# Optimization experiments

Measured on AMD Instinct MI355X. Metric: run time of the kernel, lower is better.

The kernel has to match this reference:

```python
import jax, jax.numpy as jnp
import numpy as np

B, N, DIM, H, DH = 16, 1024, 768, 12, 64
SCALE = DH ** -0.5


def setup_inputs() -> dict:
    key = jax.random.key(0)
    k1, k2, k3 = jax.random.split(key, 3)
    x = jax.random.normal(k1, (B, N, DIM), dtype=jnp.float32)
    W_qkv = jax.random.normal(k2, (DIM, 3 * H * DH), dtype=jnp.float32) * (DIM ** -0.5)
    W_out = jax.random.normal(k3, (H * DH, DIM), dtype=jnp.float32) * ((H * DH) ** -0.5)
    b_out = jnp.zeros((DIM,), dtype=jnp.float32)
    # perm = [0] + random shuffle of 1..N-1 (matches module's construction)
    rng = np.random.default_rng(0)
    perm = jnp.asarray(np.concatenate([[0], rng.permutation(np.arange(1, N))]), dtype=jnp.int32)
    return {"x": x, "W_qkv": W_qkv, "W_out": W_out, "b_out": b_out, "perm": perm}


def reference(x, W_qkv, W_out, b_out, perm):
    # QKV projection: [b, n, 3*h*d]
    qkv = jnp.einsum('bnd,de->bne', x, W_qkv)
    q, k, v = jnp.split(qkv, 3, axis=-1)
    # [b, n, h*d] -> [b, h, n, d]
    reshape = lambda t: t.reshape(B, N, H, DH).transpose(0, 2, 1, 3)
    q, k, v = reshape(q), reshape(k), reshape(v)
    # permute query rows
    q = q[:, :, perm]
    dots = jnp.einsum('bhqd,bhkd->bhqk', q, k) * SCALE
    attn = jax.nn.softmax(dots, axis=-1)
    out = jnp.einsum('bhqk,bhkd->bhqd', attn, v)
    out = out.transpose(0, 2, 1, 3).reshape(B, N, H * DH)
    return jnp.einsum('bne,ed->bnd', out, W_out) + b_out
```

## Files before the change

kernel.cpp:

```cpp
#include <hip/hip_runtime.h>
#include <hip/hip_bf16.h>


typedef __bf16 bf16x8 __attribute__((ext_vector_type(8)));
typedef __bf16 bf16x4 __attribute__((ext_vector_type(4)));
typedef float  f32x4  __attribute__((ext_vector_type(4)));

__device__ __forceinline__ f32x4 mfma16(bf16x8 a, bf16x8 b, f32x4 c) {
    return __builtin_amdgcn_mfma_f32_16x16x32_bf16(a, b, c, 0, 0, 0);
}

__device__ __forceinline__ void async16(const void* g, void* l) {
    __builtin_amdgcn_global_load_lds(
        (const __attribute__((address_space(1))) unsigned int*)g,
        (__attribute__((address_space(3))) unsigned int*)l,
        16, 0, 0);
}

__global__ void detect_dtype(const unsigned short* __restrict__ raw, int* __restrict__ flag) {
    __shared__ int cnt;
    if (threadIdx.x == 0) cnt = 0;
    __syncthreads();
    int local = 0;
    for (int i = threadIdx.x; i < 2048; i += 256) {
        unsigned e = (raw[i] >> 7) & 0xFFu;
        if (e >= 0xC0u) local++;
    }
    atomicAdd(&cnt, local);
    __syncthreads();
    if (threadIdx.x == 0) *flag = (cnt > 16) ? 1 : 0;
}

__global__ void convert_to_bf16(const void* __restrict__ src, __bf16* __restrict__ dst,
                                int n4, const int* __restrict__ flag) {
    const int f = *flag;
    int i = blockIdx.x * blockDim.x + threadIdx.x;
    const int stride = gridDim.x * blockDim.x;
    if (f) {
        const float4* s = (const float4*)src;
        for (; i < n4; i += stride) {
            float4 v = s[i];
            bf16x4 o;
            o[0] = (__bf16)v.x; o[1] = (__bf16)v.y;
            o[2] = (__bf16)v.z; o[3] = (__bf16)v.w;
            *(bf16x4*)&dst[(size_t)i * 4] = o;
        }
    } else {
        const ushort4* s = (const ushort4*)src;
        for (; i < n4; i += stride) *(ushort4*)&dst[(size_t)i * 4] = s[i];
    }
}

__global__ void transpose_dyn(const void* __restrict__ in, __bf16* __restrict__ out,
                              int R, int C, const int* __restrict__ flag) {
    __shared__ __bf16 tile[64][65];
    const int f = *flag;
    const int c0 = blockIdx.x * 64, r0 = blockIdx.y * 64;
    const int tx = threadIdx.x, ty = threadIdx.y;
#pragma unroll
    for (int k = 0; k < 16; ++k) {
        int r = ty + 4 * k;
        size_t idx = (size_t)(r0 + r) * C + c0 + tx;
        tile[r][tx] = f ? (__bf16)((const float*)in)[idx] : ((const __bf16*)in)[idx];
    }
    __syncthreads();
#pragma unroll
    for (int k = 0; k < 16; ++k) {
        int cc = ty + 4 * k;
        out[(size_t)(c0 + cc) * R + r0 + tx] = tile[tx][cc];
    }
}

__global__ void transpose_v(const __bf16* __restrict__ qkv, __bf16* __restrict__ vt) {
    __shared__ __bf16 tile[64][65];
    const int bh = blockIdx.y;
    const int b = bh / 12, h = bh % 12;
    const int n0 = blockIdx.x * 64;
    const int tx = threadIdx.x, ty = threadIdx.y;
#pragma unroll
    for (int k = 0; k < 16; ++k) {
        int n = ty + 4 * k;
        tile[n][tx] = qkv[((size_t)b * 1024 + n0 + n) * 2304 + 1536 + h * 64 + tx];
    }
    __syncthreads();
#pragma unroll
    for (int k = 0; k < 16; ++k) {
        int d = ty + 4 * k;
        vt[((size_t)bh * 64 + d) * 1024 + n0 + tx] = tile[tx][d];
    }
}

#define GMFMA16()                                                       \
    acc[0][0] = mfma16(af0, bf0, acc[0][0]);                            \
    acc[0][1] = mfma16(af0, bf1, acc[0][1]);                            \
    acc[0][2] = mfma16(af0, bf2, acc[0][2]);                            \
    acc[0][3] = mfma16(af0, bf3, acc[0][3]);                            \
    acc[1][0] = mfma16(af1, bf0, acc[1][0]);                            \
    acc[1][1] = mfma16(af1, bf1, acc[1][1]);                            \
    acc[1][2] = mfma16(af1, bf2, acc[1][2]);                            \
    acc[1][3] = mfma16(af1, bf3, acc[1][3]);                            \
    acc[2][0] = mfma16(af2, bf0, acc[2][0]);                            \
    acc[2][1] = mfma16(af2, bf1, acc[2][1]);                            \
    acc[2][2] = mfma16(af2, bf2, acc[2][2]);                            \
    acc[2][3] = mfma16(af2, bf3, acc[2][3]);                            \
    acc[3][0] = mfma16(af3, bf0, acc[3][0]);                            \
    acc[3][1] = mfma16(af3, bf1, acc[3][1]);                            \
    acc[3][2] = mfma16(af3, bf2, acc[3][2]);                            \
    acc[3][3] = mfma16(af3, bf3, acc[3][3])

#define GTILE(RD, ST, DO_STAGE, DO_SYNC) do {                           \
    if (DO_STAGE) {                                                     \
        async16(gA0, smem + (ST) + stA0);                               \
        async16(gA1, smem + (ST) + stA1);                               \
        async16(gB0, smem + (ST) + 8192 + stA0);                        \
        async16(gB1, smem + (ST) + 8192 + stA1);                        \
        gA0 += 32; gA1 += 32; gB0 += 32; gB1 += 32;                     \
    }                                                                   \
    bf16x8 af0 = *(const bf16x8*)(smem + (RD) + aoff0);                 \
    bf16x8 af1 = *(const bf16x8*)(smem + (RD) + aoff1);                 \
    bf16x8 af2 = *(const bf16x8*)(smem + (RD) + aoff2);                 \
    bf16x8 af3 = *(const bf16x8*)(smem + (RD) + aoff3);                 \
    bf16x8 bf0 = *(const bf16x8*)(smem + (RD) + boff0);                 \
    bf16x8 bf1 = *(const bf16x8*)(smem + (RD) + boff1);                 \
    bf16x8 bf2 = *(const bf16x8*)(smem + (RD) + boff2);                 \
    bf16x8 bf3 = *(const bf16x8*)(smem + (RD) + boff3);                 \
    GMFMA16();                                                          \
    if (DO_SYNC) {                                                      \
        asm volatile("s_waitcnt vmcnt(0)" ::: "memory");                \
        __builtin_amdgcn_s_barrier();                                   \
    }                                                                   \
} while (0)

template <int MODE>
__global__ __launch_bounds__(256, 3)
void gemm_bt(const __bf16* __restrict__ A, int lda,
             const __bf16* __restrict__ Bt,
             const void* __restrict__ bias,
             void* __restrict__ Cout, int ldc,
             int K, const int* __restrict__ flag) {
    __shared__ __align__(16) char smem[32768];
    const int tid  = threadIdx.x;
    const int wid  = tid >> 6;
    const int lane = tid & 63;
    const int quad = lane >> 4;
    const int l15  = lane & 15;

    const int bm = blockIdx.x * 128;
    const int bn = blockIdx.y * 128;

    const int wm = (wid & 1) * 64;
    const int wn = (wid >> 1) * 64;
    const int srow  = lane >> 2;
    const int sslot = lane & 3;

    const int rA0 = wid * 16 + srow;
    const int rA1 = 64 + wid * 16 + srow;
    const __bf16* gA0 = A  + (size_t)(bm + rA0) * lda + ((sslot ^ ((rA0 >> 1) & 3)) << 3);
    const __bf16* gA1 = A  + (size_t)(bm + rA1) * lda + ((sslot ^ ((rA1 >> 1) & 3)) << 3);
    const __bf16* gB0 = Bt + (size_t)(bn + rA0) * K   + ((sslot ^ ((rA0 >> 1) & 3)) << 3);
    const __bf16* gB1 = Bt + (size_t)(bn + rA1) * K   + ((sslot ^ ((rA1 >> 1) & 3)) << 3);
    const int stA0 = (wid * 16) * 64;
    const int stA1 = (64 + wid * 16) * 64;

    const int rf0 = wm + 0 * 16 + l15, rf1 = wm + 1 * 16 + l15;
    const int rf2 = wm + 2 * 16 + l15, rf3 = wm + 3 * 16 + l15;
    const int aoff0 = rf0 * 64 + ((quad ^ ((rf0 >> 1) & 3)) * 16);
    const int aoff1 = rf1 * 64 + ((quad ^ ((rf1 >> 1) & 3)) * 16);
    const int aoff2 = rf2 * 64 + ((quad ^ ((rf2 >> 1) & 3)) * 16);
    const int aoff3 = rf3 * 64 + ((quad ^ ((rf3 >> 1) & 3)) * 16);
    const int rg0 = wn + 0 * 16 + l15, rg1 = wn + 1 * 16 + l15;
    const int rg2 = wn + 2 * 16 + l15, rg3 = wn + 3 * 16 + l15;
    const int boff0 = 8192 + rg0 * 64 + ((quad ^ ((rg0 >> 1) & 3)) * 16);
    const int boff1 = 8192 + rg1 * 64 + ((quad ^ ((rg1 >> 1) & 3)) * 16);
    const int boff2 = 8192 + rg2 * 64 + ((quad ^ ((rg2 >> 1) & 3)) * 16);
    const int boff3 = 8192 + rg3 * 64 + ((quad ^ ((rg3 >> 1) & 3)) * 16);

    f32x4 acc[4][4];
#pragma unroll
    for (int i = 0; i < 4; ++i)
#pragma unroll
        for (int j = 0; j < 4; ++j) acc[i][j] = (f32x4)0.0f;

    async16(gA0, smem + stA0);
    async16(gA1, smem + stA1);
    async16(gB0, smem + 8192 + stA0);
    async16(gB1, smem + 8192 + stA1);
    gA0 += 32; gA1 += 32; gB0 += 32; gB1 += 32;
    asm volatile("s_waitcnt vmcnt(0)" ::: "memory");
    __builtin_amdgcn_s_barrier();

    const int nkt = K >> 5;
#pragma unroll 1
    for (int kt = 0; kt < nkt; kt += 2) {
        const bool more = (kt + 2 < nkt);
        GTILE(0,     16384, true, true);
        GTILE(16384, 0,     more, more);
    }

    const int f = (MODE == 1) ? *flag : 0;
    if (MODE == 1) {
#pragma unroll
        for (int ni = 0; ni < 4; ++ni) {
            int col = bn + wn + ni * 16 + l15;
            float bv = f ? ((const float*)bias)[col] : (float)((const __bf16*)bias)[col];
#pragma unroll
            for (int mi = 0; mi < 4; ++mi)
#pragma unroll
                for (int rg = 0; rg < 4; ++rg) acc[mi][ni][rg] += bv;
        }
    }

    if (MODE == 0 || !f) {
        __bf16* cs = (__bf16*)smem;
#pragma unroll
        for (int c = 0; c < 4; ++c) {
            __syncthreads();
            if (wm == (c >> 1) * 64) {
                int mb = (c & 1) * 2;
#pragma unroll
                for (int mloc = 0; mloc < 2; ++mloc) {
                    int rowc = mloc * 16 + quad * 4;
#pragma unroll
                    for (int ni = 0; ni < 4; ++ni) {
                        int col = wn + ni * 16 + l15;
#pragma unroll
                        for (int rg = 0; rg < 4; ++rg)
                            cs[(rowc + rg) * 136 + col] = (__bf16)acc[mb + mloc][ni][rg];
                    }
                }
            }
            __syncthreads();
#pragma unroll
            for (int p = 0; p < 2; ++p) {
                int row  = p * 16 + (tid >> 4);
                int colc = tid & 15;
                bf16x8 v = *(const bf16x8*)&cs[row * 136 + colc * 8];
                *(bf16x8*)((__bf16*)Cout + (size_t)(bm + c * 32 + row) * ldc + bn + colc * 8) = v;
            }
        }
    } else {
        float* cs = (float*)smem;
#pragma unroll
        for (int c = 0; c < 8; ++c) {
            __syncthreads();
            if (wm == (c >> 2) * 64) {
                int mi = c & 3;
                int rowc = quad * 4;
#pragma unroll
                for (int ni = 0; ni < 4; ++ni) {
                    int col = wn + ni * 16 + l15;
#pragma unroll
                    for (int rg = 0; rg < 4; ++rg)
                        cs[(rowc + rg) * 132 + col] = acc[mi][ni][rg];
                }
            }
            __syncthreads();
#pragma unroll
            for (int p = 0; p < 2; ++p) {
                int row  = p * 8 + (tid >> 5);
                int colc = tid & 31;
                float4 v = *(const float4*)&cs[row * 132 + colc * 4];
                *(float4*)((float*)Cout + (size_t)(bm + c * 16 + row) * ldc + bn + colc * 4) = v;
            }
        }
    }
}

__global__ __launch_bounds__(256, 2)
void attn(const __bf16* qkv, const __bf16* __restrict__ vt,
          const int* __restrict__ perm, __bf16* O, int ldo) {
    __shared__ __align__(16) char smem[38912];
    __bf16* Qs = (__bf16*)smem;
    __bf16* Ks = (__bf16*)smem;
    __bf16* Vs = (__bf16*)(smem + 8192);
    __bf16* Ps = (__bf16*)(smem + 16384);

    const int tid  = threadIdx.x;
    const int wid  = tid >> 6;
    const int lane = tid & 63;
    const int quad = lane >> 4;
    const int l15  = lane & 15;
    const int bh = blockIdx.x;
    const int q0 = blockIdx.y * 128;
    const int b = bh / 12, h = bh % 12;
    const size_t row_base = (size_t)b * 1024;
    const int qcol = h * 64;
    const int kcol = 768 + h * 64;
    const int srow8  = lane >> 3;
    const int sslot8 = lane & 7;
    __bf16* Pw = Ps + wid * (32 * 88);

#pragma unroll
    for (int is = 0; is < 4; ++is) {
        int r = is * 32 + wid * 8 + srow8;
        int gr = perm[q0 + r];
        int chunk = sslot8 ^ (r & 7);
        async16(qkv + (row_base + gr) * 2304 + qcol + chunk * 8,
                &Qs[(is * 32 + wid * 8) * 64]);
    }
    __syncthreads();

    bf16x8 qf[2][2];
#pragma unroll
    for (int mi = 0; mi < 2; ++mi) {
        int r = wid * 32 + mi * 16 + l15;
#pragma unroll
        for (int ks = 0; ks < 2; ++ks)
            qf[mi][ks] = *(const bf16x8*)&Qs[r * 64 + (((ks * 4 + quad) ^ (r & 7)) * 8)];
    }

    const int off0 = l15 * 64 + (((0 * 4 + quad) ^ (l15 & 7)) * 8);
    const int off1 = l15 * 64 + (((1 * 4 + quad) ^ (l15 & 7)) * 8);
    const int pwb  = l15 * 88 + quad * 4;
    const int pfb  = l15 * 88 + quad * 8;

    const int rK = wid * 8 + srow8;
    const int ck = sslot8 ^ (rK & 7);
    const __bf16* kg0 = qkv + (row_base + rK) * 2304 + kcol + ck * 8;
    const __bf16* kg1 = kg0 + (size_t)32 * 2304;
    const __bf16* vg0 = vt + ((size_t)bh * 64 + rK) * 1024 + ck * 8;
    const __bf16* vg1 = vg0 + (size_t)32 * 1024;

    f32x4 acco[2][4];
#pragma unroll
    for (int mi = 0; mi < 2; ++mi)
#pragma unroll
        for (int ni = 0; ni < 4; ++ni) acco[mi][ni] = (f32x4)0.0f;
    float lsum[2] = {0.0f, 0.0f};

    const float cfac = 0.125f * 1.44269504088896340736f;

    for (int kt = 0; kt < 16; ++kt) {
        __syncthreads();
        async16(kg0, &Ks[(wid * 8) * 64]);
        async16(kg1, &Ks[(32 + wid * 8) * 64]);
        async16(vg0, &Vs[(wid * 8) * 64]);
        async16(vg1, &Vs[(32 + wid * 8) * 64]);
        kg0 += (size_t)64 * 2304;
        kg1 += (size_t)64 * 2304;
        vg0 += 64;
        vg1 += 64;
        __syncthreads();

#pragma unroll
        for (int half = 0; half < 2; ++half) {
            f32x4 accs[2][2];
#pragma unroll
            for (int ki = 0; ki < 2; ++ki)
#pragma unroll
                for (int mi = 0; mi < 2; ++mi) accs[ki][mi] = (f32x4)0.0f;
#pragma unroll
            for (int ks = 0; ks < 2; ++ks) {
                const int off = ks ? off1 : off0;
                bf16x8 kf0 = *(const bf16x8*)&Ks[(half * 2 + 0) * 1024 + off];
                bf16x8 kf1 = *(const bf16x8*)&Ks[(half * 2 + 1) * 1024 + off];
                accs[0][0] = mfma16(kf0, qf[0][ks], accs[0][0]);
                accs[0][1] = mfma16(kf0, qf[1][ks], accs[0][1]);
                accs[1][0] = mfma16(kf1, qf[0][ks], accs[1][0]);
                accs[1][1] = mfma16(kf1, qf[1][ks], accs[1][1]);
            }

#pragma unroll
            for (int ki = 0; ki < 2; ++ki)
#pragma unroll
                for (int mi = 0; mi < 2; ++mi) {
                    bf16x4 pk;
                    float s0 = __builtin_amdgcn_exp2f(accs[ki][mi][0] * cfac - 8.0f);
                    float s1 = __builtin_amdgcn_exp2f(accs[ki][mi][1] * cfac - 8.0f);
                    float s2 = __builtin_amdgcn_exp2f(accs[ki][mi][2] * cfac - 8.0f);
                    float s3 = __builtin_amdgcn_exp2f(accs[ki][mi][3] * cfac - 8.0f);
                    pk[0] = (__bf16)s0; pk[1] = (__bf16)s1;
                    pk[2] = (__bf16)s2; pk[3] = (__bf16)s3;
                    lsum[mi] += (s0 + s1) + (s2 + s3);
                    *(bf16x4*)&Pw[pwb + mi * 1408 + (half * 2 + ki) * 16] = pk;
                }

            {
                bf16x8 pf0 = *(const bf16x8*)&Pw[pfb + 0 * 1408 + half * 32];
                bf16x8 pf1 = *(const bf16x8*)&Pw[pfb + 1 * 1408 + half * 32];
                const int offv = half ? off1 : off0;
#pragma unroll
                for (int ni = 0; ni < 4; ++ni) {
                    bf16x8 vf = *(const bf16x8*)&Vs[ni * 1024 + offv];
                    acco[0][ni] = mfma16(pf0, vf, acco[0][ni]);
                    acco[1][ni] = mfma16(pf1, vf, acco[1][ni]);
                }
            }
        }
    }

#pragma unroll
    for (int off = 16; off < 64; off <<= 1) {
        lsum[0] += __shfl_xor(lsum[0], off, 64);
        lsum[1] += __shfl_xor(lsum[1], off, 64);
    }

#pragma unroll
    for (int mi = 0; mi < 2; ++mi) {
#pragma unroll
        for (int rg = 0; rg < 4; ++rg) {
            float inv = 1.0f / __shfl(lsum[mi], quad * 4 + rg, 64);
            int orow = q0 + wid * 32 + mi * 16 + quad * 4 + rg;
#pragma unroll
            for (int ni = 0; ni < 4; ++ni) {
                int ocol = h * 64 + ni * 16 + l15;
                O[(row_base + orow) * (size_t)ldo + ocol] = (__bf16)(acco[mi][ni][rg] * inv);
            }
        }
    }
}

extern "C" void kernel_launch(void* const* d_in, const int* in_sizes, int n_in,
                              void* d_out, int out_size, void* d_ws, size_t ws_size,
                              hipStream_t stream) {
    (void)in_sizes; (void)n_in; (void)out_size; (void)ws_size;
    const void* x_raw    = d_in[0];
    const void* Wqkv_raw = d_in[1];
    const void* Wout_raw = d_in[2];
    const void* bout_raw = d_in[3];
    const int*  perm     = (const int*)d_in[4];

    char* ws = (char*)d_ws;
    int*    flag = (int*)ws;
    __bf16* Xc   = (__bf16*)(ws + 256);
    __bf16* QKV  = (__bf16*)(ws + 25166080);
    __bf16* Vt   = (__bf16*)(ws + 100663552);
    __bf16* Wqt  = (__bf16*)(ws + 125829376);
    __bf16* Wot  = (__bf16*)(ws + 129368320);
    __bf16* Obuf = QKV + 1536;

    detect_dtype<<<1, 256, 0, stream>>>((const unsigned short*)x_raw, flag);
    convert_to_bf16<<<2048, 256, 0, stream>>>(x_raw, Xc, 16384 * 768 / 4, flag);
    transpose_dyn<<<dim3(36, 12), dim3(64, 4), 0, stream>>>(Wqkv_raw, Wqt, 768, 2304, flag);
    transpose_dyn<<<dim3(12, 12), dim3(64, 4), 0, stream>>>(Wout_raw, Wot, 768, 768, flag);
    gemm_bt<0><<<dim3(128, 18), 256, 0, stream>>>(Xc, 768, Wqt, nullptr, QKV, 2304, 768, nullptr);
    transpose_v<<<dim3(16, 192), dim3(64, 4), 0, stream>>>(QKV, Vt);
    attn<<<dim3(192, 8), 256, 0, stream>>>(QKV, Vt, perm, Obuf, 2304);
    gemm_bt<1><<<dim3(128, 6), 256, 0, stream>>>(Obuf, 2304, Wot, bout_raw, d_out, 768, 768, flag);
}
```

Before: 217.6 us.

## Fuse V transpose into QKV GEMM epilogue and double-buffer attention K/V loads

The QKV GEMM now writes the V columns straight into a transposed Vt buffer from its accumulators, which removes the separate transpose_v kernel and its extra round trip of V through global memory. The attention kernel gets double-buffered K/V shared-memory stages, so the next tile's async loads overlap with compute on the current tile, and each tile now needs one barrier instead of two. In exchange, attention uses more LDS, which may lower occupancy, and the Vt stores from the GEMM are narrow strided writes.

```diff
diff --git a/kernel.cpp b/kernel.cpp
--- a/kernel.cpp
+++ b/kernel.cpp
@@ -68,25 +68,6 @@
     for (int k = 0; k < 16; ++k) {
         int cc = ty + 4 * k;
         out[(size_t)(c0 + cc) * R + r0 + tx] = tile[tx][cc];
-    }
-}
-
-__global__ void transpose_v(const __bf16* __restrict__ qkv, __bf16* __restrict__ vt) {
-    __shared__ __bf16 tile[64][65];
-    const int bh = blockIdx.y;
-    const int b = bh / 12, h = bh % 12;
-    const int n0 = blockIdx.x * 64;
-    const int tx = threadIdx.x, ty = threadIdx.y;
-#pragma unroll
-    for (int k = 0; k < 16; ++k) {
-        int n = ty + 4 * k;
-        tile[n][tx] = qkv[((size_t)b * 1024 + n0 + n) * 2304 + 1536 + h * 64 + tx];
-    }
-    __syncthreads();
-#pragma unroll
-    for (int k = 0; k < 16; ++k) {
-        int d = ty + 4 * k;
-        vt[((size_t)bh * 64 + d) * 1024 + n0 + tx] = tile[tx][d];
     }
 }
 
@@ -137,7 +118,8 @@
              const __bf16* __restrict__ Bt,
              const void* __restrict__ bias,
              void* __restrict__ Cout, int ldc,
-             int K, const int* __restrict__ flag) {
+             int K, const int* __restrict__ flag,
+             __bf16* __restrict__ vt) {
     __shared__ __align__(16) char smem[32768];
     const int tid  = threadIdx.x;
     const int wid  = tid >> 6;
@@ -197,6 +179,25 @@
         GTILE(16384, 0,     more, more);
     }
 
+    if (MODE == 0 && bn >= 1536) {
+        const int bq = bm >> 10;
+        const int n0 = (bm & 1023) + wm + quad * 4;
+        const int colb = bn - 1536 + wn;
+#pragma unroll
+        for (int mi = 0; mi < 4; ++mi)
+#pragma unroll
+            for (int ni = 0; ni < 4; ++ni) {
+                int col = colb + ni * 16 + l15;
+                bf16x4 v;
+                v[0] = (__bf16)acc[mi][ni][0];
+                v[1] = (__bf16)acc[mi][ni][1];
+                v[2] = (__bf16)acc[mi][ni][2];
+                v[3] = (__bf16)acc[mi][ni][3];
+                *(bf16x4*)&vt[((size_t)bq * 768 + col) * 1024 + n0 + mi * 16] = v;
+            }
+        return;
+    }
+
     const int f = (MODE == 1) ? *flag : 0;
     if (MODE == 1) {
 #pragma unroll
@@ -269,11 +270,9 @@
 __global__ __launch_bounds__(256, 2)
 void attn(const __bf16* qkv, const __bf16* __restrict__ vt,
           const int* __restrict__ perm, __bf16* O, int ldo) {
-    __shared__ __align__(16) char smem[38912];
+    __shared__ __align__(16) char smem[55296];
     __bf16* Qs = (__bf16*)smem;
-    __bf16* Ks = (__bf16*)smem;
-    __bf16* Vs = (__bf16*)(smem + 8192);
-    __bf16* Ps = (__bf16*)(smem + 16384);
+    __bf16* Ps = (__bf16*)(smem + 32768);
 
     const int tid  = threadIdx.x;
     const int wid  = tid >> 6;
@@ -308,6 +307,9 @@
         for (int ks = 0; ks < 2; ++ks)
             qf[mi][ks] = *(const bf16x8*)&Qs[r * 64 + (((ks * 4 + quad) ^ (r & 7)) * 8)];
     }
+    asm volatile("s_waitcnt lgkmcnt(0)" ::: "memory");
+    __builtin_amdgcn_sched_barrier(0);
+    __builtin_amdgcn_s_barrier();
 
     const int off0 = l15 * 64 + (((0 * 4 + quad) ^ (l15 & 7)) * 8);
     const int off1 = l15 * 64 + (((1 * 4 + quad) ^ (l15 & 7)) * 8);
@@ -330,18 +332,16 @@
 
     const float cfac = 0.125f * 1.44269504088896340736f;
 
-    for (int kt = 0; kt < 16; ++kt) {
-        __syncthreads();
-        async16(kg0, &Ks[(wid * 8) * 64]);
-        async16(kg1, &Ks[(32 + wid * 8) * 64]);
-        async16(vg0, &Vs[(wid * 8) * 64]);
-        async16(vg1, &Vs[(32 + wid * 8) * 64]);
-        kg0 += (size_t)64 * 2304;
-        kg1 += (size_t)64 * 2304;
-        vg0 += 64;
-        vg1 += 64;
-        __syncthreads();
-
+#define ASTAGE(KB, VB) do {                                             \
+        async16(kg0, smem + (KB) + wid * 1024);                         \
+        async16(kg1, smem + (KB) + 4096 + wid * 1024);                  \
+        async16(vg0, smem + (VB) + wid * 1024);                         \
+        async16(vg1, smem + (VB) + 4096 + wid * 1024);                  \
+        kg0 += (size_t)64 * 2304; kg1 += (size_t)64 * 2304;             \
+        vg0 += 64; vg1 += 64;                                           \
+    } while (0)
+
+    auto compute = [&](const __bf16* Kb, const __bf16* Vb) {
 #pragma unroll
         for (int half = 0; half < 2; ++half) {
             f32x4 accs[2][2];
@@ -352,8 +352,8 @@
 #pragma unroll
             for (int ks = 0; ks < 2; ++ks) {
                 const int off = ks ? off1 : off0;
-                bf16x8 kf0 = *(const bf16x8*)&Ks[(half * 2 + 0) * 1024 + off];
-                bf16x8 kf1 = *(const bf16x8*)&Ks[(half * 2 + 1) * 1024 + off];
+                bf16x8 kf0 = *(const bf16x8*)&Kb[(half * 2 + 0) * 1024 + off];
+                bf16x8 kf1 = *(const bf16x8*)&Kb[(half * 2 + 1) * 1024 + off];
                 accs[0][0] = mfma16(kf0, qf[0][ks], accs[0][0]);
                 accs[0][1] = mfma16(kf0, qf[1][ks], accs[0][1]);
                 accs[1][0] = mfma16(kf1, qf[0][ks], accs[1][0]);
@@ -381,13 +381,28 @@
                 const int offv = half ? off1 : off0;
 #pragma unroll
                 for (int ni = 0; ni < 4; ++ni) {
-                    bf16x8 vf = *(const bf16x8*)&Vs[ni * 1024 + offv];
+                    bf16x8 vf = *(const bf16x8*)&Vb[ni * 1024 + offv];
                     acco[0][ni] = mfma16(pf0, vf, acco[0][ni]);
                     acco[1][ni] = mfma16(pf1, vf, acco[1][ni]);
                 }
             }
         }
-    }
+    };
+
+    ASTAGE(0, 16384);
+
+#pragma unroll 1
+    for (int kt2 = 0; kt2 < 8; ++kt2) {
+        asm volatile("s_waitcnt vmcnt(0)" ::: "memory");
+        __builtin_amdgcn_s_barrier();
+        ASTAGE(8192, 16384 + 8192);
+        compute((const __bf16*)smem, (const __bf16*)(smem + 16384));
+        asm volatile("s_waitcnt vmcnt(0)" ::: "memory");
+        __builtin_amdgcn_s_barrier();
+        if (kt2 < 7) ASTAGE(0, 16384);
+        compute((const __bf16*)(smem + 8192), (const __bf16*)(smem + 16384 + 8192));
+    }
+#undef ASTAGE
 
 #pragma unroll
     for (int off = 16; off < 64; off <<= 1) {
@@ -433,8 +448,7 @@
     convert_to_bf16<<<2048, 256, 0, stream>>>(x_raw, Xc, 16384 * 768 / 4, flag);
     transpose_dyn<<<dim3(36, 12), dim3(64, 4), 0, stream>>>(Wqkv_raw, Wqt, 768, 2304, flag);
     transpose_dyn<<<dim3(12, 12), dim3(64, 4), 0, stream>>>(Wout_raw, Wot, 768, 768, flag);
-    gemm_bt<0><<<dim3(128, 18), 256, 0, stream>>>(Xc, 768, Wqt, nullptr, QKV, 2304, 768, nullptr);
-    transpose_v<<<dim3(16, 192), dim3(64, 4), 0, stream>>>(QKV, Vt);
+    gemm_bt<0><<<dim3(128, 18), 256, 0, stream>>>(Xc, 768, Wqt, nullptr, QKV, 2304, 768, nullptr, Vt);
     attn<<<dim3(192, 8), 256, 0, stream>>>(QKV, Vt, perm, Obuf, 2304);
-    gemm_bt<1><<<dim3(128, 6), 256, 0, stream>>>(Obuf, 2304, Wot, bout_raw, d_out, 768, 768, flag);
-}
+    gemm_bt<1><<<dim3(128, 6), 256, 0, stream>>>(Obuf, 2304, Wot, bout_raw, d_out, 768, 768, flag, nullptr);
+}
```

Result: faster. 209.8 us (-3.6%).
